# Optimization experiments

Hardware: AMD Instinct MI355X
Metric: run time of the kernel (lower is better)

Reference implementation:

```python
import jax, jax.numpy as jnp
import numpy as np

N_EMBD = 1024
N_HEAD = 16
HEAD_DIM = N_EMBD // N_HEAD

def setup_inputs() -> dict:
    key = jax.random.key(0)
    ks = jax.random.split(key, 5)
    B, T, C = 2, 2048, N_EMBD
    s = 1.0 / np.sqrt(C)
    x = jax.random.normal(ks[0], (B, T, C), dtype=jnp.float32)
    W_qkv = jax.random.normal(ks[1], (C, 3 * C), dtype=jnp.float32) * s
    b_qkv = jax.random.normal(ks[2], (3 * C,), dtype=jnp.float32) * 0.02
    W_o = jax.random.normal(ks[3], (C, C), dtype=jnp.float32) * s
    b_o = jax.random.normal(ks[4], (C,), dtype=jnp.float32) * 0.02
    return {"x": x, "W_qkv": W_qkv, "b_qkv": b_qkv, "W_o": W_o, "b_o": b_o}

def reference(x, W_qkv, b_qkv, W_o, b_o):
    B, T, C = x.shape
    H, D = N_HEAD, HEAD_DIM
    scale = 1.0 / np.sqrt(D)
    qkv = jnp.einsum('btc,cf->btf', x, W_qkv) + b_qkv  # [B,T,3C]
    q, k, v = jnp.split(qkv, 3, axis=-1)
    # [B,H,T,D]
    q = q.reshape(B, T, H, D).transpose(0, 2, 1, 3)
    k = k.reshape(B, T, H, D).transpose(0, 2, 1, 3)
    v = v.reshape(B, T, H, D).transpose(0, 2, 1, 3)
    att = jnp.einsum('bhqd,bhkd->bhqk', q, k) * scale  # [B,H,T,T]
    causal = jnp.tril(jnp.ones((T, T), dtype=bool))
    att = jnp.where(causal[None, None], att, -jnp.inf)
    att = jax.nn.softmax(att, axis=-1)
    y = jnp.einsum('bhqk,bhkd->bhqd', att, v)  # [B,H,T,D]
    y = y.transpose(0, 2, 1, 3).reshape(B, T, C)
    return jnp.einsum('btc,cf->btf', y, W_o) + b_o
```

## Files before the change

kernel.cpp:

```cpp
#include <hip/hip_runtime.h>
#include <hip/hip_bf16.h>

#define TT 2048
#define BB 2
#define CC 1024
#define NH 16
#define HD 64

typedef __attribute__((ext_vector_type(8))) short short8;
typedef __attribute__((ext_vector_type(4))) short short4b;
typedef __attribute__((ext_vector_type(4))) float f32x4;

typedef unsigned int __attribute__((address_space(1))) ui_gas;
typedef unsigned int __attribute__((address_space(3))) ui_las;

#if __has_builtin(__builtin_amdgcn_mfma_f32_16x16x16bf16_1k)
#define PV16 1
#define VSS 4
#else
#define PV16 0
#define VSS 8
#endif

__device__ __forceinline__ float us2f(unsigned short u) {
    union { unsigned int i; float f; } v; v.i = ((unsigned int)u) << 16; return v.f;
}
__device__ __forceinline__ unsigned short f2us(float f) {
    union { float f; unsigned int i; } v; v.f = f;
    unsigned int i = v.i;
    unsigned int lsb = (i >> 16) & 1u;
    i += 0x7fffu + lsb;
    return (unsigned short)(i >> 16);
}
__device__ __forceinline__ unsigned int pack2_trunc(float a, float b) {
    union { float f; unsigned int u; } x, y; x.f = a; y.f = b;
    return (y.u & 0xffff0000u) | (x.u >> 16);
}

__device__ __forceinline__ void gl_lds16(const unsigned short* g, unsigned short* l) {
    __builtin_amdgcn_global_load_lds((const ui_gas*)g, (ui_las*)l, 16, 0, 0);
}

__device__ __forceinline__ float4 load4(const void* p, size_t i, int isbf) {
    if (isbf) {
        ushort4 u = *reinterpret_cast<const ushort4*>((const unsigned short*)p + i);
        return make_float4(us2f(u.x), us2f(u.y), us2f(u.z), us2f(u.w));
    } else {
        return *reinterpret_cast<const float4*>((const float*)p + i);
    }
}
__device__ __forceinline__ float load1(const void* p, size_t i, int isbf) {
    return isbf ? us2f(((const unsigned short*)p)[i]) : ((const float*)p)[i];
}

__global__ __launch_bounds__(256) void prep_kernel(
    const void* __restrict__ x, const void* __restrict__ Wqkv, const void* __restrict__ Wo,
    const void* __restrict__ bqkv, const void* __restrict__ bo,
    unsigned short* __restrict__ xb, unsigned short* __restrict__ Wqkvt,
    unsigned short* __restrict__ Wot, int* __restrict__ flags)
{
    __shared__ float Ls[64 * 65];
    __shared__ int sh_isbf;
    const int t = threadIdx.x;
    const int bid = blockIdx.x;

    const void* src;
    int mode, sub;
    if (bid < 2048)      { mode = 0; sub = bid;        src = x; }
    else if (bid < 2816) { mode = 1; sub = bid - 2048; src = Wqkv; }
    else                 { mode = 2; sub = bid - 2816; src = Wo; }

    if (bid == 0 && t < 64) {
        const void* ps[5] = {x, Wqkv, bqkv, Wo, bo};
        for (int k = 0; k < 5; ++k) {
            const unsigned short* u = (const unsigned short*)ps[k];
            int bad = 0;
            #pragma unroll
            for (int j = 0; j < 4; ++j) {
                float v = us2f(u[t * 4 + j]);
                if (!(fabsf(v) < 1e4f)) bad = 1;
            }
            unsigned long long m = __ballot(bad != 0);
            if (t == 0) flags[k] = (__popcll(m) < 4) ? 1 : 0;
        }
    }
    if (t < 64) {
        const unsigned short* u = (const unsigned short*)src;
        int bad = 0;
        #pragma unroll
        for (int j = 0; j < 4; ++j) {
            float v = us2f(u[t * 4 + j]);
            if (!(fabsf(v) < 1e4f)) bad = 1;
        }
        unsigned long long m = __ballot(bad != 0);
        if (t == 0) sh_isbf = (__popcll(m) < 4) ? 1 : 0;
    }
    __syncthreads();
    const int isbf = sh_isbf;

    if (mode == 0) {
        const size_t i = ((size_t)sub * 256 + t) * 8;
        float4 a = load4(src, i, isbf);
        float4 b = load4(src, i + 4, isbf);
        alignas(16) unsigned short pk[8];
        pk[0] = f2us(a.x); pk[1] = f2us(a.y); pk[2] = f2us(a.z); pk[3] = f2us(a.w);
        pk[4] = f2us(b.x); pk[5] = f2us(b.y); pk[6] = f2us(b.z); pk[7] = f2us(b.w);
        *reinterpret_cast<uint4*>(xb + i) = *reinterpret_cast<const uint4*>(pk);
        return;
    }

    int N, Krows, n0, k0;
    unsigned short* dst;
    if (mode == 1) { N = 3 * CC; Krows = CC; dst = Wqkvt; n0 = (sub % 48) * 64; k0 = (sub / 48) * 64; }
    else           { N = CC;     Krows = CC; dst = Wot;   n0 = (sub % 16) * 64; k0 = (sub / 16) * 64; }
    {
        const int r = t >> 2, cq = (t & 3) << 4;
        #pragma unroll
        for (int i = 0; i < 4; ++i) {
            float4 v = load4(src, (size_t)(k0 + r) * N + n0 + cq + i * 4, isbf);
            Ls[r * 65 + cq + i * 4 + 0] = v.x;
            Ls[r * 65 + cq + i * 4 + 1] = v.y;
            Ls[r * 65 + cq + i * 4 + 2] = v.z;
            Ls[r * 65 + cq + i * 4 + 3] = v.w;
        }
    }
    __syncthreads();
    {
        const int c = t & 63, kg = (t >> 6) * 16;
        alignas(16) unsigned short pk[16];
        #pragma unroll
        for (int i = 0; i < 16; ++i) pk[i] = f2us(Ls[(kg + i) * 65 + c]);
        unsigned short* d = dst + (size_t)(n0 + c) * Krows + k0 + kg;
        *reinterpret_cast<uint4*>(d + 0) = *reinterpret_cast<const uint4*>(&pk[0]);
        *reinterpret_cast<uint4*>(d + 8) = *reinterpret_cast<const uint4*>(&pk[8]);
    }
}

__global__ __launch_bounds__(512, 2) void gemm_qkv(
    const unsigned short* __restrict__ A,
    const unsigned short* __restrict__ Bt,
    const void* __restrict__ bias, unsigned short* __restrict__ Cq,
    unsigned short* __restrict__ Vt, const int* __restrict__ flags)
{
    constexpr int K = CC;
    constexpr int QBM = 256, QBN = 192;
    constexpr int ASL = QBM / 16;
    constexpr int TOT = ASL + QBN / 16;
    constexpr int TS  = QBM + 8;
    __shared__ __align__(16) unsigned short SH[QBN * TS];

    const int tid = threadIdx.x;
    const int l = tid & 63, w = tid >> 6;
    const int wm = w >> 2, wn = w & 3;
    const int lm = l & 15, lk = (l >> 4) * 8, quad = l >> 4;

    const int lin = blockIdx.y * 16 + blockIdx.x;
    const int xcd = lin & 7, loc = lin >> 3;
    const int bx = (xcd & 3) * 4 + (loc & 3);
    const int by = (xcd >> 2) * 8 + (loc >> 2);
    const int bm = by * QBM, bn = bx * QBN;

    f32x4 acc[8][3];
    #pragma unroll
    for (int i = 0; i < 8; ++i)
        #pragma unroll
        for (int j = 0; j < 3; ++j) acc[i][j] = (f32x4){0.f, 0.f, 0.f, 0.f};

    auto stage = [&](int bb, int k0) {
        unsigned short* base = SH + bb * (TOT * 512);
        if (w < 4) {
            #pragma unroll
            for (int s = 0; s < 4; ++s) {
                const int slab = w * 4 + s;
                gl_lds16(A + (size_t)(bm + slab * 16 + lm) * K + k0 + lk,
                         base + slab * 512);
            }
        } else {
            #pragma unroll
            for (int s = 0; s < 3; ++s) {
                const int slab = ASL + (w - 4) * 3 + s;
                gl_lds16(Bt + (size_t)(bn + (slab - ASL) * 16 + lm) * K + k0 + lk,
                         base + slab * 512);
            }
        }
    };

    auto compute = [&](int bb) {
        const unsigned short* base = SH + bb * (TOT * 512);
        short8 af[8], bf[3];
        #pragma unroll
        for (int i = 0; i < 8; ++i)
            af[i] = *reinterpret_cast<const short8*>(&base[(wm * 8 + i) * 512 + l * 8]);
        #pragma unroll
        for (int j = 0; j < 3; ++j)
            bf[j] = *reinterpret_cast<const short8*>(&base[(ASL + wn * 3 + j) * 512 + l * 8]);
        #pragma unroll
        for (int i = 0; i < 8; ++i)
            #pragma unroll
            for (int j = 0; j < 3; ++j)
                acc[i][j] = __builtin_amdgcn_mfma_f32_16x16x32_bf16(af[i], bf[j], acc[i][j], 0, 0, 0);
    };

    const int nt = K >> 5;
    stage(0, 0);
    stage(1, 32);
    if (w < 4) asm volatile("s_waitcnt vmcnt(4)" ::: "memory");
    else       asm volatile("s_waitcnt vmcnt(3)" ::: "memory");
    __builtin_amdgcn_sched_barrier(0);
    __builtin_amdgcn_s_barrier();

    for (int t = 0; t < nt; ++t) {
        if (t + 2 < nt) stage((t + 2) % 3, (t + 2) << 5);
        compute(t % 3);
        if (t + 2 < nt) {
            if (w < 4) asm volatile("s_waitcnt vmcnt(4)" ::: "memory");
            else       asm volatile("s_waitcnt vmcnt(3)" ::: "memory");
        } else {
            asm volatile("s_waitcnt vmcnt(0)" ::: "memory");
        }
        __builtin_amdgcn_sched_barrier(0);
        __builtin_amdgcn_s_barrier();
    }

    const int bias_bf = flags[2];
    float bv[3];
    #pragma unroll
    for (int j = 0; j < 3; ++j) bv[j] = load1(bias, bn + (wn * 3 + j) * 16 + lm, bias_bf);

    const int vstart = 2 * CC - bn;

    #pragma unroll
    for (int i = 0; i < 8; ++i) {
        #pragma unroll
        for (int r = 0; r < 4; ++r) {
            const int rl = wm * 128 + i * 16 + quad * 4 + r;
            const int row = bm + rl;
            #pragma unroll
            for (int j = 0; j < 3; ++j) {
                const int cl2 = (wn * 3 + j) * 16 + lm;
                const unsigned short us = f2us(acc[i][j][r] + bv[j]);
                Cq[(size_t)row * (3 * CC) + bn + cl2] = us;
                if (cl2 >= vstart) SH[cl2 * TS + rl] = us;
            }
        }
    }

    if (vstart < QBN) {
        __syncthreads();
        const int v0 = vstart > 0 ? vstart : 0;
        const int vcnt = QBN - v0;
        if (tid < vcnt * 2) {
            const int cl = v0 + (tid >> 1), rq = tid & 1;
            const int cc2 = bn + cl - 2 * CC;
            const int hh = cc2 >> 6, dd = cc2 & 63;
            const int bq = bm >> 11;
            const int tk = (bm & (TT - 1)) + rq * 128;
            unsigned short* dst = Vt + ((size_t)(bq * NH + hh) * HD + dd) * TT + tk;
            const unsigned short* srcp = &SH[cl * TS + rq * 128];
            #pragma unroll
            for (int k = 0; k < 16; ++k)
                *(uint4*)(dst + k * 8) = *(const uint4*)(srcp + k * 8);
        }
    }
}

template<int WM, int WN, int NWM, int NWN, int SWZ, bool VTE>
__global__ __launch_bounds__(256) void gemm_mfma(
    const unsigned short* __restrict__ A,
    const unsigned short* __restrict__ Bt,
    const void* __restrict__ bias, void* __restrict__ C,
    unsigned short* __restrict__ Vt,
    int M, int N, int K,
    const int* __restrict__ flags, int biasfi, int cfi)
{
    constexpr int BM = WM * 16 * NWM, BN = WN * 16 * NWN;
    constexpr int ASL = BM / 16, BSL = BN / 16;
    constexpr int TOT = ASL + BSL;
    constexpr int PW  = TOT / 4;

    __shared__ __align__(16) unsigned short SH[3][TOT * 512];

    const int tid = threadIdx.x;
    const int l  = tid & 63;
    const int w  = tid >> 6;
    const int wm = w / NWN, wn = w % NWN;
    const int lm = l & 15;
    const int lk = (l >> 4) * 8;
    const int quad = l >> 4;

    int bx, by;
    if constexpr (SWZ == 4) {
        const int lin = blockIdx.y * 8 + blockIdx.x;
        const int xcd = lin & 7, loc = lin >> 3;
        bx = loc & 7;
        by = xcd * 4 + (loc >> 3);
    } else {
        bx = blockIdx.x; by = blockIdx.y;
    }
    const int bm = by * BM, bn = bx * BN;

    f32x4 acc[WM][WN];
    #pragma unroll
    for (int i = 0; i < WM; ++i)
        #pragma unroll
        for (int j = 0; j < WN; ++j) acc[i][j] = (f32x4){0.f, 0.f, 0.f, 0.f};

    auto stage = [&](int bb, int k0) {
        #pragma unroll
        for (int s = 0; s < PW; ++s) {
            const int slab = w * PW + s;
            const unsigned short* src;
            if (slab < ASL) src = A  + (size_t)(bm + slab * 16 + lm) * K + k0 + lk;
            else            src = Bt + (size_t)(bn + (slab - ASL) * 16 + lm) * K + k0 + lk;
            gl_lds16(src, &SH[bb][slab * 512]);
        }
    };

    auto compute = [&](int bb) {
        short8 af[WM], bf[WN];
        #pragma unroll
        for (int i = 0; i < WM; ++i)
            af[i] = *reinterpret_cast<const short8*>(&SH[bb][(wm * WM + i) * 512 + l * 8]);
        #pragma unroll
        for (int j = 0; j < WN; ++j)
            bf[j] = *reinterpret_cast<const short8*>(&SH[bb][(ASL + wn * WN + j) * 512 + l * 8]);
        #pragma unroll
        for (int i = 0; i < WM; ++i)
            #pragma unroll
            for (int j = 0; j < WN; ++j)
                acc[i][j] = __builtin_amdgcn_mfma_f32_16x16x32_bf16(af[i], bf[j], acc[i][j], 0, 0, 0);
    };

    const int nt = K >> 5;
    stage(0, 0);
    stage(1, 32);
    asm volatile("s_waitcnt vmcnt(%0)" :: "n"(PW) : "memory");
    __builtin_amdgcn_sched_barrier(0);
    __builtin_amdgcn_s_barrier();

    for (int t = 0; t < nt; ++t) {
        if (t + 2 < nt) stage((t + 2) % 3, (t + 2) << 5);
        compute(t % 3);
        if (t + 2 < nt) {
            asm volatile("s_waitcnt vmcnt(%0)" :: "n"(PW) : "memory");
        } else {
            asm volatile("s_waitcnt vmcnt(0)" ::: "memory");
        }
        __builtin_amdgcn_sched_barrier(0);
        __builtin_amdgcn_s_barrier();
    }

    const int bias_bf = (biasfi >= 0) ? flags[biasfi] : 0;
    const int c_bf    = (cfi >= 0) ? flags[cfi] : ((cfi == -2) ? 1 : 0);
    float bv[WN];
    #pragma unroll
    for (int j = 0; j < WN; ++j) bv[j] = load1(bias, bn + (WN * wn + j) * 16 + lm, bias_bf);

    #pragma unroll
    for (int i = 0; i < WM; ++i) {
        #pragma unroll
        for (int r = 0; r < 4; ++r) {
            const int row = bm + (WM * wm + i) * 16 + quad * 4 + r;
            #pragma unroll
            for (int j = 0; j < WN; ++j) {
                const int col = bn + (WN * wn + j) * 16 + lm;
                const float val = acc[i][j][r] + bv[j];
                if (c_bf) ((unsigned short*)C)[(size_t)row * N + col] = f2us(val);
                else      ((float*)C)[(size_t)row * N + col] = val;
            }
        }
    }
}

__global__ __launch_bounds__(256) void attn_mfma(
    const unsigned short* __restrict__ qkv,
    const unsigned short* __restrict__ Vt,
    unsigned short* __restrict__ y)
{
    __shared__ __align__(16) unsigned short Ksh[8 * 512];
    __shared__ __align__(16) unsigned short Vsh[1039 * VSS];

    const int tid = threadIdx.x;
    const int l   = tid & 63;
    const int w   = tid >> 6;
    const int quad = l >> 4;
    const int col  = l & 15;

    const int n  = blockIdx.x;
    const int g  = n >> 3;
    const int bh = (n & 7) * 4 + (g & 3);
    const int i  = g >> 2;
    const int tA = i, tB = 31 - i;
    const int b  = bh >> 4, h = bh & 15;

#if !PV16
    for (int ss = tid; ss < 1039; ss += 256)
        *(uint2*)(&Vsh[ss * 8 + 4]) = make_uint2(0u, 0u);
#endif

    const float QSCALE = 0.18033688f;
    short8 qfA[2], qfB[2];
    #pragma unroll
    for (int t2 = 0; t2 < 2; ++t2) {
        const int qt = t2 ? tB : tA;
        short8* qf = t2 ? qfB : qfA;
        const int token = qt * 64 + w * 16 + col;
        const unsigned short* qrow = qkv + (size_t)(b * TT + token) * 3 * CC + h * HD;
        #pragma unroll
        for (int ks = 0; ks < 2; ++ks) {
            ushort4 u0 = *(const ushort4*)(qrow + ks * 32 + quad * 8);
            ushort4 u1 = *(const ushort4*)(qrow + ks * 32 + quad * 8 + 4);
            alignas(16) unsigned short pk[8];
            pk[0] = f2us(us2f(u0.x) * QSCALE);
            pk[1] = f2us(us2f(u0.y) * QSCALE);
            pk[2] = f2us(us2f(u0.z) * QSCALE);
            pk[3] = f2us(us2f(u0.w) * QSCALE);
            pk[4] = f2us(us2f(u1.x) * QSCALE);
            pk[5] = f2us(us2f(u1.y) * QSCALE);
            pk[6] = f2us(us2f(u1.z) * QSCALE);
            pk[7] = f2us(us2f(u1.w) * QSCALE);
            qf[ks] = *(const short8*)pk;
        }
    }

    f32x4 oA[4], oB[4];
    #pragma unroll
    for (int nb = 0; nb < 4; ++nb) {
        oA[nb] = (f32x4){0.f, 0.f, 0.f, 0.f};
        oB[nb] = (f32x4){0.f, 0.f, 0.f, 0.f};
    }
    float lAc = 0.f, lBc = 0.f;

    const unsigned short* kbase = qkv + (size_t)b * TT * 3 * CC + CC + h * HD;
    const unsigned short* vbase = Vt + (size_t)bh * HD * TT;

    const int vd = tid >> 2, vg0 = (tid & 3) * 4;

    uint4 rk[2], rv[2];
    auto issue_loads = [&](int kt) {
        const unsigned short* ksrc = kbase + (size_t)(kt * 64 + l) * 3 * CC;
        #pragma unroll
        for (int c2 = 0; c2 < 2; ++c2) {
            const int c = 2 * w + c2;
            rk[c2] = *(const uint4*)(ksrc + c * 8);
        }
        const unsigned short* vsrc = vbase + (size_t)vd * TT + kt * 64 + vg0 * 4;
        rv[0] = *(const uint4*)(vsrc + 0);
        rv[1] = *(const uint4*)(vsrc + 8);
    };
    auto write_lds = [&]() {
        #pragma unroll
        for (int c2 = 0; c2 < 2; ++c2) {
            const int c = 2 * w + c2;
            const int ks = c >> 2, q = c & 3;
            const int slot = ((quad * 2 + ks) * 64 + q * 16 + col) * 8;
            *(uint4*)(&Ksh[slot]) = rk[c2];
        }
        *(uint2*)(&Vsh[((vg0 + 0) * 65 + vd) * VSS]) = make_uint2(rv[0].x, rv[0].y);
        *(uint2*)(&Vsh[((vg0 + 1) * 65 + vd) * VSS]) = make_uint2(rv[0].z, rv[0].w);
        *(uint2*)(&Vsh[((vg0 + 2) * 65 + vd) * VSS]) = make_uint2(rv[1].x, rv[1].y);
        *(uint2*)(&Vsh[((vg0 + 3) * 65 + vd) * VSS]) = make_uint2(rv[1].z, rv[1].w);
    };

    auto step = [&](const short8* qf, f32x4* o, float& l_i, bool diag) {
        f32x4 st[4];
        #pragma unroll
        for (int nb = 0; nb < 4; ++nb) {
            f32x4 acc = {0.f, 0.f, 0.f, 0.f};
            #pragma unroll
            for (int ks = 0; ks < 2; ++ks) {
                short8 kf = *(const short8*)(&Ksh[((nb * 2 + ks) * 64 + l) * 8]);
                acc = __builtin_amdgcn_mfma_f32_16x16x32_bf16(kf, qf[ks], acc, 0, 0, 0);
            }
            st[nb] = acc;
        }
        float pv[4][4];
        float rs = 0.f;
        #pragma unroll
        for (int nb = 0; nb < 4; ++nb)
            #pragma unroll
            for (int r = 0; r < 4; ++r) {
                float v = st[nb][r];
                if (diag && (nb * 16 + quad * 4 + r > w * 16 + col)) v = -3e38f;
                float p = __builtin_exp2f(v);
                pv[nb][r] = p;
                rs += p;
            }
        rs += __shfl_xor(rs, 16);
        rs += __shfl_xor(rs, 32);
        l_i += rs;
#if PV16
        short4b pf[4];
        #pragma unroll
        for (int nbk = 0; nbk < 4; ++nbk) {
            union { short4b s; unsigned int u[2]; } pk;
            pk.u[0] = pack2_trunc(pv[nbk][0], pv[nbk][1]);
            pk.u[1] = pack2_trunc(pv[nbk][2], pv[nbk][3]);
            pf[nbk] = pk.s;
        }
        #pragma unroll
        for (int nbd = 0; nbd < 4; ++nbd)
            #pragma unroll
            for (int nbk = 0; nbk < 4; ++nbk) {
                short4b vf = *(const short4b*)(&Vsh[((nbk * 4 + quad) * 65 + nbd * 16 + col) * VSS]);
                o[nbd] = __builtin_amdgcn_mfma_f32_16x16x16bf16_1k(pf[nbk], vf, o[nbd], 0, 0, 0);
            }
#else
        short8 pf[4];
        #pragma unroll
        for (int nbk = 0; nbk < 4; ++nbk) {
            union { short8 s; unsigned int u[4]; } pk;
            pk.u[0] = pack2_trunc(pv[nbk][0], pv[nbk][1]);
            pk.u[1] = pack2_trunc(pv[nbk][2], pv[nbk][3]);
            pk.u[2] = 0u; pk.u[3] = 0u;
            pf[nbk] = pk.s;
        }
        #pragma unroll
        for (int nbd = 0; nbd < 4; ++nbd)
            #pragma unroll
            for (int nbk = 0; nbk < 4; ++nbk) {
                short8 vf = *(const short8*)(&Vsh[((nbk * 4 + quad) * 65 + nbd * 16 + col) * VSS]);
                o[nbd] = __builtin_amdgcn_mfma_f32_16x16x32_bf16(pf[nbk], vf, o[nbd], 0, 0, 0);
            }
#endif
    };

    issue_loads(0);
    for (int kt = 0; kt <= tB; ++kt) {
        write_lds();
        __syncthreads();
        if (kt < tB) issue_loads(kt + 1);
        step(qfB, oB, lBc, kt == tB);
        if (kt <= tA) step(qfA, oA, lAc, kt == tA);
        __syncthreads();
    }

    #pragma unroll
    for (int t2 = 0; t2 < 2; ++t2) {
        const int qt = t2 ? tB : tA;
        f32x4* o = t2 ? oB : oA;
        const float inv = 1.f / (t2 ? lBc : lAc);
        float invr[4];
        #pragma unroll
        for (int r = 0; r < 4; ++r) invr[r] = __shfl(inv, quad * 4 + r);
        #pragma unroll
        for (int nb = 0; nb < 4; ++nb)
            #pragma unroll
            for (int r = 0; r < 4; ++r) {
                int token = qt * 64 + w * 16 + quad * 4 + r;
                y[(size_t)(b * TT + token) * CC + h * HD + nb * 16 + col] = f2us(o[nb][r] * invr[r]);
            }
    }
}

extern "C" void kernel_launch(void* const* d_in, const int* in_sizes, int n_in,
                              void* d_out, int out_size, void* d_ws, size_t ws_size,
                              hipStream_t stream) {
    const int M = BB * TT;

    char* ws = (char*)d_ws;
    int*            flags = (int*)ws;                         ws += 256;
    unsigned short* xb    = (unsigned short*)ws;              ws += (size_t)M * CC * 2;
    unsigned short* Wqkvt = (unsigned short*)ws;              ws += (size_t)3 * CC * CC * 2;
    unsigned short* Wot   = (unsigned short*)ws;              ws += (size_t)CC * CC * 2;
    unsigned short* qkv   = (unsigned short*)ws;              ws += (size_t)M * 3 * CC * 2;
    unsigned short* Vt    = (unsigned short*)ws;              ws += (size_t)BB * NH * HD * TT * 2;
    unsigned short* y     = (unsigned short*)ws;

    prep_kernel<<<3072, 256, 0, stream>>>(d_in[0], d_in[1], d_in[3], d_in[2], d_in[4],
                                          xb, Wqkvt, Wot, flags);

    gemm_qkv<<<dim3(16, 16), 512, 0, stream>>>(xb, Wqkvt, d_in[2], qkv, Vt, flags);

    attn_mfma<<<512, 256, 0, stream>>>(qkv, Vt, y);

    gemm_mfma<4, 4, 2, 2, 4, false><<<dim3(CC / 128, M / 128), 256, 0, stream>>>(
        y, Wot, d_in[4], d_out, nullptr, M, CC, CC, flags, 4, 0);
}
```

Baseline: 206.4 us.

## Process four query tiles per attention block to reuse K/V tiles

Each attention block now handles four query tiles (i, 15-i, 16+i, 31-i) of one batch-head instead of two, so every K/V tile loaded into shared memory is reused by up to four query tiles. The grid drops from 512 to 256 blocks, roughly halving K/V global loads and LDS staging per query. In exchange, per-thread register use grows (four sets of Q fragments and accumulators), which may lower occupancy. With 256 blocks, a 256-CU device gets about one block per CU and little latency hiding.

```diff
diff --git a/kernel.cpp b/kernel.cpp
--- a/kernel.cpp
+++ b/kernel.cpp
@@ -387,10 +387,9 @@
     const int col  = l & 15;
 
     const int n  = blockIdx.x;
-    const int g  = n >> 3;
-    const int bh = (n & 7) * 4 + (g & 3);
-    const int i  = g >> 2;
-    const int tA = i, tB = 31 - i;
+    const int bh = n & 31;
+    const int i  = n >> 5;
+    const int tq0 = 31 - i, tq1 = 16 + i, tq2 = 15 - i, tq3 = i;
     const int b  = bh >> 4, h = bh & 15;
 
 #if !PV16
@@ -399,37 +398,37 @@
 #endif
 
     const float QSCALE = 0.18033688f;
-    short8 qfA[2], qfB[2];
-    #pragma unroll
-    for (int t2 = 0; t2 < 2; ++t2) {
-        const int qt = t2 ? tB : tA;
-        short8* qf = t2 ? qfB : qfA;
-        const int token = qt * 64 + w * 16 + col;
-        const unsigned short* qrow = qkv + (size_t)(b * TT + token) * 3 * CC + h * HD;
-        #pragma unroll
-        for (int ks = 0; ks < 2; ++ks) {
-            ushort4 u0 = *(const ushort4*)(qrow + ks * 32 + quad * 8);
-            ushort4 u1 = *(const ushort4*)(qrow + ks * 32 + quad * 8 + 4);
-            alignas(16) unsigned short pk[8];
-            pk[0] = f2us(us2f(u0.x) * QSCALE);
-            pk[1] = f2us(us2f(u0.y) * QSCALE);
-            pk[2] = f2us(us2f(u0.z) * QSCALE);
-            pk[3] = f2us(us2f(u0.w) * QSCALE);
-            pk[4] = f2us(us2f(u1.x) * QSCALE);
-            pk[5] = f2us(us2f(u1.y) * QSCALE);
-            pk[6] = f2us(us2f(u1.z) * QSCALE);
-            pk[7] = f2us(us2f(u1.w) * QSCALE);
-            qf[ks] = *(const short8*)pk;
-        }
-    }
-
-    f32x4 oA[4], oB[4];
-    #pragma unroll
-    for (int nb = 0; nb < 4; ++nb) {
-        oA[nb] = (f32x4){0.f, 0.f, 0.f, 0.f};
-        oB[nb] = (f32x4){0.f, 0.f, 0.f, 0.f};
-    }
-    float lAc = 0.f, lBc = 0.f;
+    short8 qf[4][2];
+    {
+        const int tqs[4] = {tq0, tq1, tq2, tq3};
+        #pragma unroll
+        for (int s = 0; s < 4; ++s) {
+            const int token = tqs[s] * 64 + w * 16 + col;
+            const unsigned short* qrow = qkv + (size_t)(b * TT + token) * 3 * CC + h * HD;
+            #pragma unroll
+            for (int ks = 0; ks < 2; ++ks) {
+                ushort4 u0 = *(const ushort4*)(qrow + ks * 32 + quad * 8);
+                ushort4 u1 = *(const ushort4*)(qrow + ks * 32 + quad * 8 + 4);
+                alignas(16) unsigned short pk[8];
+                pk[0] = f2us(us2f(u0.x) * QSCALE);
+                pk[1] = f2us(us2f(u0.y) * QSCALE);
+                pk[2] = f2us(us2f(u0.z) * QSCALE);
+                pk[3] = f2us(us2f(u0.w) * QSCALE);
+                pk[4] = f2us(us2f(u1.x) * QSCALE);
+                pk[5] = f2us(us2f(u1.y) * QSCALE);
+                pk[6] = f2us(us2f(u1.z) * QSCALE);
+                pk[7] = f2us(us2f(u1.w) * QSCALE);
+                qf[s][ks] = *(const short8*)pk;
+            }
+        }
+    }
+
+    f32x4 o[4][4];
+    float lc[4] = {0.f, 0.f, 0.f, 0.f};
+    #pragma unroll
+    for (int s = 0; s < 4; ++s)
+        #pragma unroll
+        for (int nb = 0; nb < 4; ++nb) o[s][nb] = (f32x4){0.f, 0.f, 0.f, 0.f};
 
     const unsigned short* kbase = qkv + (size_t)b * TT * 3 * CC + CC + h * HD;
     const unsigned short* vbase = Vt + (size_t)bh * HD * TT;
@@ -462,7 +461,7 @@
         *(uint2*)(&Vsh[((vg0 + 3) * 65 + vd) * VSS]) = make_uint2(rv[1].z, rv[1].w);
     };
 
-    auto step = [&](const short8* qf, f32x4* o, float& l_i, bool diag) {
+    auto step = [&](const short8* qfs, f32x4* os, float& l_i, bool diag) {
         f32x4 st[4];
         #pragma unroll
         for (int nb = 0; nb < 4; ++nb) {
@@ -470,7 +469,7 @@
             #pragma unroll
             for (int ks = 0; ks < 2; ++ks) {
                 short8 kf = *(const short8*)(&Ksh[((nb * 2 + ks) * 64 + l) * 8]);
-                acc = __builtin_amdgcn_mfma_f32_16x16x32_bf16(kf, qf[ks], acc, 0, 0, 0);
+                acc = __builtin_amdgcn_mfma_f32_16x16x32_bf16(kf, qfs[ks], acc, 0, 0, 0);
             }
             st[nb] = acc;
         }
@@ -503,7 +502,7 @@
             #pragma unroll
             for (int nbk = 0; nbk < 4; ++nbk) {
                 short4b vf = *(const short4b*)(&Vsh[((nbk * 4 + quad) * 65 + nbd * 16 + col) * VSS]);
-                o[nbd] = __builtin_amdgcn_mfma_f32_16x16x16bf16_1k(pf[nbk], vf, o[nbd], 0, 0, 0);
+                os[nbd] = __builtin_amdgcn_mfma_f32_16x16x16bf16_1k(pf[nbk], vf, os[nbd], 0, 0, 0);
             }
 #else
         short8 pf[4];
@@ -520,36 +519,39 @@
             #pragma unroll
             for (int nbk = 0; nbk < 4; ++nbk) {
                 short8 vf = *(const short8*)(&Vsh[((nbk * 4 + quad) * 65 + nbd * 16 + col) * VSS]);
-                o[nbd] = __builtin_amdgcn_mfma_f32_16x16x32_bf16(pf[nbk], vf, o[nbd], 0, 0, 0);
+                os[nbd] = __builtin_amdgcn_mfma_f32_16x16x32_bf16(pf[nbk], vf, os[nbd], 0, 0, 0);
             }
 #endif
     };
 
     issue_loads(0);
-    for (int kt = 0; kt <= tB; ++kt) {
+    for (int kt = 0; kt <= tq0; ++kt) {
         write_lds();
         __syncthreads();
-        if (kt < tB) issue_loads(kt + 1);
-        step(qfB, oB, lBc, kt == tB);
-        if (kt <= tA) step(qfA, oA, lAc, kt == tA);
+        if (kt < tq0) issue_loads(kt + 1);
+        step(qf[0], o[0], lc[0], kt == tq0);
+        if (kt <= tq1) step(qf[1], o[1], lc[1], kt == tq1);
+        if (kt <= tq2) step(qf[2], o[2], lc[2], kt == tq2);
+        if (kt <= tq3) step(qf[3], o[3], lc[3], kt == tq3);
         __syncthreads();
     }
 
-    #pragma unroll
-    for (int t2 = 0; t2 < 2; ++t2) {
-        const int qt = t2 ? tB : tA;
-        f32x4* o = t2 ? oB : oA;
-        const float inv = 1.f / (t2 ? lBc : lAc);
-        float invr[4];
-        #pragma unroll
-        for (int r = 0; r < 4; ++r) invr[r] = __shfl(inv, quad * 4 + r);
-        #pragma unroll
-        for (int nb = 0; nb < 4; ++nb)
-            #pragma unroll
-            for (int r = 0; r < 4; ++r) {
-                int token = qt * 64 + w * 16 + quad * 4 + r;
-                y[(size_t)(b * TT + token) * CC + h * HD + nb * 16 + col] = f2us(o[nb][r] * invr[r]);
-            }
+    {
+        const int tqs[4] = {tq0, tq1, tq2, tq3};
+        #pragma unroll
+        for (int s = 0; s < 4; ++s) {
+            const float inv = 1.f / lc[s];
+            float invr[4];
+            #pragma unroll
+            for (int r = 0; r < 4; ++r) invr[r] = __shfl(inv, quad * 4 + r);
+            #pragma unroll
+            for (int nb = 0; nb < 4; ++nb)
+                #pragma unroll
+                for (int r = 0; r < 4; ++r) {
+                    int token = tqs[s] * 64 + w * 16 + quad * 4 + r;
+                    y[(size_t)(b * TT + token) * CC + h * HD + nb * 16 + col] = f2us(o[s][nb][r] * invr[r]);
+                }
+        }
     }
 }
 
@@ -572,7 +574,7 @@
 
     gemm_qkv<<<dim3(16, 16), 512, 0, stream>>>(xb, Wqkvt, d_in[2], qkv, Vt, flags);
 
-    attn_mfma<<<512, 256, 0, stream>>>(qkv, Vt, y);
+    attn_mfma<<<256, 256, 0, stream>>>(qkv, Vt, y);
 
     gemm_mfma<4, 4, 2, 2, 4, false><<<dim3(CC / 128, M / 128), 256, 0, stream>>>(
         y, Wot, d_in[4], d_out, nullptr, M, CC, CC, flags, 4, 0);
```

Measured after the change: 221.4 us. 7.3% more time.
